# Kernel optimization log

Measured on AMD Instinct MI355X. Metric: run time of the kernel, lower is better.

Reference implementation:

```python
import jax, jax.numpy as jnp
import numpy as np

DIM, NH, WS, SS, MLP_RATIO = 192, 6, 8, 4, 4
EPS = 1e-5


def _rel_pos_index(ws):
    coords = np.stack(np.meshgrid(np.arange(ws), np.arange(ws), indexing='ij')).reshape(2, -1)
    rel = (coords[:, :, None] - coords[:, None, :]).transpose(1, 2, 0)
    rel[:, :, 0] += ws - 1
    rel[:, :, 1] += ws - 1
    rel[:, :, 0] *= 2 * ws - 1
    return rel.sum(-1)  # (ws*ws, ws*ws) int


def _attn_mask(hp, wp, ws, ss):
    img = np.zeros((hp, wp))
    slices = (slice(0, -ws), slice(-ws, -ss), slice(-ss, None))
    cnt = 0
    for hs in slices:
        for vs in slices:
            img[hs, vs] = cnt
            cnt += 1
    mw = img.reshape(hp // ws, ws, wp // ws, ws).transpose(0, 2, 1, 3).reshape(-1, ws * ws)
    am = mw[:, None, :] - mw[:, :, None]  # (nW, N, N)
    return jnp.asarray(np.where(am != 0, -100.0, 0.0).astype(np.float32))


def _ln(x, g, b):
    mu = jnp.mean(x, axis=-1, keepdims=True)
    var = jnp.mean(jnp.square(x - mu), axis=-1, keepdims=True)
    return (x - mu) * jax.lax.rsqrt(var + EPS) * g + b


def setup_inputs():
    key = jax.random.key(0)
    ks = jax.random.split(key, 8)
    B, H, W, C = 8, 128, 128, DIM
    hid = C * MLP_RATIO
    n = lambda k, s: jax.random.normal(k, s, dtype=jnp.float32) * 0.02
    return {
        'x': jax.random.normal(ks[0], (B, H * W, C), dtype=jnp.float32),
        'h': H, 'w': W,
        'norm1_g': jnp.ones((C,), jnp.float32), 'norm1_b': jnp.zeros((C,), jnp.float32),
        'qkv_w': n(ks[1], (C, 3 * C)), 'qkv_b': jnp.zeros((3 * C,), jnp.float32),
        'proj_w': n(ks[2], (C, C)), 'proj_b': jnp.zeros((C,), jnp.float32),
        'rel_bias_table': n(ks[3], ((2 * WS - 1) ** 2, NH)),
        'norm2_g': jnp.ones((C,), jnp.float32), 'norm2_b': jnp.zeros((C,), jnp.float32),
        'fc1_w': n(ks[4], (C, hid)), 'fc1_b': jnp.zeros((hid,), jnp.float32),
        'fc2_w': n(ks[5], (hid, C)), 'fc2_b': jnp.zeros((C,), jnp.float32),
    }


def reference(x, h, w, norm1_g, norm1_b, qkv_w, qkv_b, proj_w, proj_b,
              rel_bias_table, norm2_g, norm2_b, fc1_w, fc1_b, fc2_w, fc2_b):
    B, L, C = x.shape
    ws, ss, nh = WS, SS, NH
    hd = C // nh
    scale = hd ** (-0.5)

    shortcut = x
    xg = _ln(x, norm1_g, norm1_b).reshape(B, h, w, C)

    pad_h = (-h) % ws
    pad_w = (-w) % ws
    if pad_h or pad_w:
        xg = jnp.pad(xg, ((0, 0), (0, pad_h), (0, pad_w), (0, 0)))
    hp, wp = h + pad_h, w + pad_w
    if ss > 0:
        xg = jnp.roll(xg, (-ss, -ss), axis=(1, 2))

    # window partition -> (nB, N, C)
    win = xg.reshape(B, hp // ws, ws, wp // ws, ws, C).transpose(0, 1, 3, 2, 4, 5).reshape(-1, ws * ws, C)
    nB, N, _ = win.shape

    qkv = (win @ qkv_w + qkv_b).reshape(nB, N, 3, nh, hd).transpose(2, 0, 3, 1, 4)
    q, k, v = qkv[0] * scale, qkv[1], qkv[2]  # (nB, nh, N, hd)

    attn = jnp.einsum('bhnd,bhmd->bhnm', q, k)  # (nB, nh, N, N)
    rpi = _rel_pos_index(ws)
    bias = rel_bias_table[rpi.reshape(-1)].reshape(N, N, nh).transpose(2, 0, 1)
    attn = attn + bias[None]
    if ss > 0:
        mask = _attn_mask(hp, wp, ws, ss)  # (nW, N, N)
        nW = mask.shape[0]
        attn = (attn.reshape(nB // nW, nW, nh, N, N) + mask[None, :, None]).reshape(nB, nh, N, N)
    attn = jax.nn.softmax(attn, axis=-1)

    out = jnp.einsum('bhnm,bhmd->bnhd', attn, v).reshape(nB, N, C)
    out = out @ proj_w + proj_b

    # window reverse
    out = out.reshape(B, hp // ws, wp // ws, ws, ws, C).transpose(0, 1, 3, 2, 4, 5).reshape(B, hp, wp, C)
    if ss > 0:
        out = jnp.roll(out, (ss, ss), axis=(1, 2))
    out = out[:, :h, :w].reshape(B, h * w, C)

    x = shortcut + out
    xn2 = _ln(x, norm2_g, norm2_b)
    mlp = jax.nn.gelu(xn2 @ fc1_w + fc1_b, approximate=False) @ fc2_w + fc2_b
    return x + mlp
```

## Files before the change

### kernel.cpp

```cpp
#include <hip/hip_runtime.h>

typedef unsigned short u16;
typedef unsigned int   u32;
typedef __attribute__((ext_vector_type(8))) short bf16x8;
typedef __attribute__((ext_vector_type(4))) float f32x4;

#define L_TOK   16384
#define C_DIM   192
#define HID_DIM 768

#define OFF_QKV  0
#define OFF_PROJ 110592
#define OFF_FC1  147456
#define OFF_FC2  294912
#define CVT_TOT  442368

union FragU { int4 i4; bf16x8 h8; };

#define MFMA_B16(a,b,c) __builtin_amdgcn_mfma_f32_16x16x32_bf16(a,b,c,0,0,0)

__device__ __forceinline__ u16 f2bf(float f) {
    u32 t; __builtin_memcpy(&t, &f, 4);
    t += 0x7FFFu + ((t >> 16) & 1u);
    return (u16)(t >> 16);
}

__global__ __launch_bounds__(256) void k_cvt(
    const float* __restrict__ qkvw, const float* __restrict__ projw,
    const float* __restrict__ fc1w, const float* __restrict__ fc2w,
    u16* __restrict__ ws)
{
    const int i = blockIdx.x * 256 + threadIdx.x;
    if (i >= CVT_TOT) return;
    float v;
    if (i < OFF_PROJ) {
        const int k = i % 192, tmp = i / 192;
        const int cc = tmp % 96, head = tmp / 96;
        const int grp = cc >> 5, dim = cc & 31;
        v = qkvw[(size_t)k * 576 + grp * 192 + head * 32 + dim];
    } else if (i < OFF_FC1) {
        const int idx = i - OFF_PROJ;
        const int j = idx & 31, tmp = idx >> 5;
        const int c = tmp % 192, head = tmp / 192;
        v = projw[(size_t)(head * 32 + j) * 192 + c];
    } else if (i < OFF_FC2) {
        const int idx = i - OFF_FC1;
        const int k = idx % 192, h = idx / 192;
        v = fc1w[(size_t)k * 768 + h];
    } else {
        const int idx = i - OFF_FC2;
        const int h = idx % 768, c = idx / 768;
        v = fc2w[(size_t)h * 192 + c];
    }
    ws[i] = f2bf(v);
}

__global__ __launch_bounds__(256) void k_attnproj(
    const float* __restrict__ x, const float* __restrict__ g1v, const float* __restrict__ b1v,
    const u16* __restrict__ qkvwT, const float* __restrict__ qkvb,
    const float* __restrict__ relb, const u16* __restrict__ projT, const float* __restrict__ projb,
    float* __restrict__ x1)
{
    union SmemU {
        u16 xw[64 * 200];
        struct {
            u16 qsb[64 * 40];
            u16 ksb[64 * 40];
            u16 vsbT[32 * 72];
            u16 psb[64 * 72];
            u16 oh [64 * 40];
        } s;
    };
    __shared__ __align__(16) SmemU u;
    __shared__ __align__(16) u16 wbuf[192 * 40];
    __shared__ float relbs[225 * 6];

    const int wi = blockIdx.x;
    const int b  = wi >> 8;
    const int hb = (wi >> 4) & 15;
    const int wb = wi & 15;
    const int t  = threadIdx.x;
    const int lane = t & 63, w = t >> 6;
    const int l15 = lane & 15, quad = lane >> 4;
    const bool maskon = (hb == 15) || (wb == 15);
    const f32x4 zf = {0.f, 0.f, 0.f, 0.f};

    for (int i = t; i < 225 * 6; i += 256) relbs[i] = relb[i];

    {
        const int n  = t >> 2;
        const int q4 = t & 3;
        const int r = n >> 3, c = n & 7;
        const int ho = (hb * 8 + r + 4) & 127;
        const int wo = (wb * 8 + c + 4) & 127;
        const size_t xoff = ((size_t)b * L_TOK + ho * 128 + wo) * C_DIM;
        const float* xp = x + xoff + q4 * 48;
        float f[48];
        float sum = 0.f, sq = 0.f;
        #pragma unroll
        for (int i = 0; i < 12; ++i) {
            float4 v = *(const float4*)(xp + i * 4);
            f[i*4+0]=v.x; f[i*4+1]=v.y; f[i*4+2]=v.z; f[i*4+3]=v.w;
            sum += v.x+v.y+v.z+v.w;
            sq  += v.x*v.x + v.y*v.y + v.z*v.z + v.w*v.w;
        }
        sum += __shfl_xor(sum, 1); sum += __shfl_xor(sum, 2);
        sq  += __shfl_xor(sq, 1);  sq  += __shfl_xor(sq, 2);
        const float mu = sum * (1.f / 192.f);
        const float rstd = rsqrtf(sq * (1.f / 192.f) - mu * mu + 1e-5f);
        u16* xrow = u.xw + n * 200 + q4 * 48;
        #pragma unroll
        for (int i = 0; i < 6; ++i) {
            u32 pk[4];
            #pragma unroll
            for (int j = 0; j < 4; ++j) {
                float g0 = g1v[q4*48 + i*8 + j*2],     b0 = b1v[q4*48 + i*8 + j*2];
                float g1 = g1v[q4*48 + i*8 + j*2 + 1], b1 = b1v[q4*48 + i*8 + j*2 + 1];
                float y0 = (f[i*8+j*2]   - mu) * rstd * g0 + b0;
                float y1 = (f[i*8+j*2+1] - mu) * rstd * g1 + b1;
                pk[j] = (u32)f2bf(y0) | (((u32)f2bf(y1)) << 16);
            }
            *(int4*)(xrow + i * 8) = make_int4((int)pk[0], (int)pk[1], (int)pk[2], (int)pk[3]);
        }
    }
    __syncthreads();

    FragU afrag[6];
    #pragma unroll
    for (int kk = 0; kk < 6; ++kk)
        afrag[kk].i4 = *(const int4*)(u.xw + (w*16 + l15) * 200 + kk*32 + quad*8);

    const int qrow0 = w*16 + quad*4;

    f32x4 acc2[12];
    #pragma unroll
    for (int nt = 0; nt < 12; ++nt) acc2[nt] = zf;

    for (int head = 0; head < 6; ++head) {
        f32x4 accq[6];
        #pragma unroll
        for (int nt = 0; nt < 6; ++nt) accq[nt] = zf;

        for (int kc = 0; kc < 3; ++kc) {
            __syncthreads();
            {
                const u16* src = qkvwT + (size_t)head * (96 * 192) + kc * 64;
                #pragma unroll
                for (int i = 0; i < 3; ++i) {
                    const int e = t + i * 256;
                    const int cc = e >> 3, seg = e & 7;
                    *(int4*)(wbuf + cc*72 + seg*8) =
                        *(const int4*)(src + cc*192 + seg*8);
                }
            }
            __syncthreads();
            #pragma unroll
            for (int s = 0; s < 2; ++s) {
                #pragma unroll
                for (int nt = 0; nt < 6; ++nt) {
                    FragU bf_;
                    bf_.i4 = *(const int4*)(wbuf + (nt*16 + l15)*72 + s*32 + quad*8);
                    accq[nt] = MFMA_B16(afrag[kc*2 + s].h8, bf_.h8, accq[nt]);
                }
            }
        }
        #pragma unroll
        for (int nt = 0; nt < 6; ++nt) {
            const int grp = nt >> 1;
            const int dim = (nt & 1)*16 + l15;
            const float bias = qkvb[grp*192 + head*32 + dim];
            float vv[4];
            #pragma unroll
            for (int rg = 0; rg < 4; ++rg) vv[rg] = accq[nt][rg] + bias;
            if (grp == 0) {
                #pragma unroll
                for (int rg = 0; rg < 4; ++rg)
                    u.s.qsb[(qrow0 + rg)*40 + dim] = f2bf(vv[rg] * 0.17677669529663687f);
            } else if (grp == 1) {
                #pragma unroll
                for (int rg = 0; rg < 4; ++rg)
                    u.s.ksb[(qrow0 + rg)*40 + dim] = f2bf(vv[rg]);
            } else {
                u32 lo = (u32)f2bf(vv[0]) | (((u32)f2bf(vv[1])) << 16);
                u32 hi = (u32)f2bf(vv[2]) | (((u32)f2bf(vv[3])) << 16);
                *(uint2*)&u.s.vsbT[dim*72 + w*16 + quad*4] = make_uint2(lo, hi);
            }
        }
        __syncthreads();

        FragU qf; qf.i4 = *(const int4*)(u.s.qsb + (w*16 + l15)*40 + quad*8);
        f32x4 sv[4];
        #pragma unroll
        for (int nt = 0; nt < 4; ++nt) {
            FragU kf; kf.i4 = *(const int4*)(u.s.ksb + (nt*16 + l15)*40 + quad*8);
            sv[nt] = MFMA_B16(qf.h8, kf.h8, zf);
        }
        const int kr_ = l15 >> 3, kc2 = l15 & 7;
        #pragma unroll
        for (int rg = 0; rg < 4; ++rg) {
            const int qm = qrow0 + rg;
            const int qr = qm >> 3, qc = qm & 7;
            #pragma unroll
            for (int nt = 0; nt < 4; ++nt) {
                const int kr = nt*2 + kr_;
                sv[nt][rg] += relbs[((qr - kr + 7)*15 + (qc - kc2 + 7))*6 + head];
            }
        }
        if (maskon) {
            #pragma unroll
            for (int rg = 0; rg < 4; ++rg) {
                const int qm = qrow0 + rg;
                const int qr = qm >> 3, qc = qm & 7;
                const int regq = ((hb == 15) ? (qr < 4 ? 1 : 2) : 0) * 3
                               + ((wb == 15) ? (qc < 4 ? 1 : 2) : 0);
                #pragma unroll
                for (int nt = 0; nt < 4; ++nt) {
                    const int kr = nt*2 + kr_;
                    const int regk = ((hb == 15) ? (kr < 4 ? 1 : 2) : 0) * 3
                                   + ((wb == 15) ? (kc2 < 4 ? 1 : 2) : 0);
                    if (regq != regk) sv[nt][rg] -= 100.f;
                }
            }
        }
        #pragma unroll
        for (int rg = 0; rg < 4; ++rg) {
            float mx = fmaxf(fmaxf(sv[0][rg], sv[1][rg]), fmaxf(sv[2][rg], sv[3][rg]));
            mx = fmaxf(mx, __shfl_xor(mx, 1));
            mx = fmaxf(mx, __shfl_xor(mx, 2));
            mx = fmaxf(mx, __shfl_xor(mx, 4));
            mx = fmaxf(mx, __shfl_xor(mx, 8));
            float s0 = 0.f;
            #pragma unroll
            for (int nt = 0; nt < 4; ++nt) { sv[nt][rg] = __expf(sv[nt][rg] - mx); s0 += sv[nt][rg]; }
            s0 += __shfl_xor(s0, 1); s0 += __shfl_xor(s0, 2);
            s0 += __shfl_xor(s0, 4); s0 += __shfl_xor(s0, 8);
            const float inv = 1.f / s0;
            #pragma unroll
            for (int nt = 0; nt < 4; ++nt)
                u.s.psb[(qrow0 + rg)*72 + nt*16 + l15] = f2bf(sv[nt][rg] * inv);
        }

        FragU pa0, pa1;
        pa0.i4 = *(const int4*)(u.s.psb + (w*16 + l15)*72 + quad*8);
        pa1.i4 = *(const int4*)(u.s.psb + (w*16 + l15)*72 + 32 + quad*8);
        f32x4 ov[2];
        ov[0] = zf; ov[1] = zf;
        #pragma unroll
        for (int ntv = 0; ntv < 2; ++ntv) {
            FragU vb0, vb1;
            vb0.i4 = *(const int4*)(u.s.vsbT + (ntv*16 + l15)*72 + quad*8);
            vb1.i4 = *(const int4*)(u.s.vsbT + (ntv*16 + l15)*72 + 32 + quad*8);
            ov[ntv] = MFMA_B16(pa0.h8, vb0.h8, ov[ntv]);
            ov[ntv] = MFMA_B16(pa1.h8, vb1.h8, ov[ntv]);
        }
        #pragma unroll
        for (int ntv = 0; ntv < 2; ++ntv)
            #pragma unroll
            for (int rg = 0; rg < 4; ++rg)
                u.s.oh[(qrow0 + rg)*40 + ntv*16 + l15] = f2bf(ov[ntv][rg]);

        {
            const u16* src = projT + (size_t)head * (192 * 32);
            #pragma unroll
            for (int i = 0; i < 3; ++i) {
                const int e = t + i * 256;
                const int c = e >> 2, seg = e & 3;
                *(int4*)(wbuf + c*40 + seg*8) =
                    *(const int4*)(src + c*32 + seg*8);
            }
        }
        __syncthreads();
        FragU ao; ao.i4 = *(const int4*)(u.s.oh + (w*16 + l15)*40 + quad*8);
        #pragma unroll
        for (int nt = 0; nt < 12; ++nt) {
            FragU bp; bp.i4 = *(const int4*)(wbuf + (nt*16 + l15)*40 + quad*8);
            acc2[nt] = MFMA_B16(ao.h8, bp.h8, acc2[nt]);
        }
    }

    {
        float pb[12];
        #pragma unroll
        for (int nt = 0; nt < 12; ++nt) pb[nt] = projb[nt*16 + l15];
        #pragma unroll
        for (int rg = 0; rg < 4; ++rg) {
            const int tok = qrow0 + rg;
            const int tr = tok >> 3, tc = tok & 7;
            const int ho2 = (hb * 8 + tr + 4) & 127;
            const int wo2 = (wb * 8 + tc + 4) & 127;
            const size_t base = ((size_t)b * L_TOK + ho2 * 128 + wo2) * C_DIM;
            #pragma unroll
            for (int nt = 0; nt < 12; ++nt) {
                const int col = nt*16 + l15;
                x1[base + col] = acc2[nt][rg] + pb[nt] + x[base + col];
            }
        }
    }
}

__global__ __launch_bounds__(256, 2) void k_mlp(
    const float* x1, const float* __restrict__ g2v, const float* __restrict__ b2v,
    const u16* __restrict__ fc1wT, const float* __restrict__ fc1b,
    const u16* __restrict__ fc2wT, const float* __restrict__ fc2b,
    float* out)
{
    union SmemU {
        u16 xn[128 * 200];
        u16 hbuf[128 * 104];
    };
    __shared__ __align__(16) SmemU u;
    __shared__ __align__(16) u16 wT[192 * 40];

    const int blk = blockIdx.x;
    const int t = threadIdx.x;
    const size_t row0 = (size_t)blk * 128;
    const int lane = t & 63, w = t >> 6;
    const int l15 = lane & 15, quad = lane >> 4;
    const f32x4 zf = {0.f, 0.f, 0.f, 0.f};

    #pragma unroll
    for (int tk = 0; tk < 2; ++tk) {
        const int nn = t >> 2, q4 = t & 3;
        const int tok = tk * 64 + nn;
        const float* xp = x1 + (row0 + tok) * C_DIM + q4 * 48;
        float f[48];
        float sum = 0.f, sq = 0.f;
        #pragma unroll
        for (int i = 0; i < 12; ++i) {
            float4 v = *(const float4*)(xp + i * 4);
            f[i*4+0]=v.x; f[i*4+1]=v.y; f[i*4+2]=v.z; f[i*4+3]=v.w;
            sum += v.x+v.y+v.z+v.w;
            sq  += v.x*v.x + v.y*v.y + v.z*v.z + v.w*v.w;
        }
        sum += __shfl_xor(sum,1); sum += __shfl_xor(sum,2);
        sq  += __shfl_xor(sq,1);  sq  += __shfl_xor(sq,2);
        const float mu = sum * (1.f/192.f);
        const float rstd = rsqrtf(sq * (1.f/192.f) - mu*mu + 1e-5f);
        u16* xrow = u.xn + tok * 200 + q4 * 48;
        #pragma unroll
        for (int i = 0; i < 6; ++i) {
            u32 pk[4];
            #pragma unroll
            for (int j = 0; j < 4; ++j) {
                float g0 = g2v[q4*48 + i*8 + j*2],     b0 = b2v[q4*48 + i*8 + j*2];
                float g1 = g2v[q4*48 + i*8 + j*2 + 1], b1 = b2v[q4*48 + i*8 + j*2 + 1];
                float y0 = (f[i*8+j*2]   - mu) * rstd * g0 + b0;
                float y1 = (f[i*8+j*2+1] - mu) * rstd * g1 + b1;
                pk[j] = (u32)f2bf(y0) | (((u32)f2bf(y1)) << 16);
            }
            *(int4*)(xrow + i*8) = make_int4((int)pk[0], (int)pk[1], (int)pk[2], (int)pk[3]);
        }
    }
    __syncthreads();

    FragU afrag[2][6];
    #pragma unroll
    for (int mt = 0; mt < 2; ++mt)
        #pragma unroll
        for (int kk = 0; kk < 6; ++kk)
            afrag[mt][kk].i4 = *(const int4*)(u.xn + (mt*64 + w*16 + l15) * 200 + kk*32 + quad*8);

    f32x4 acc2[2][12];
    #pragma unroll
    for (int mt = 0; mt < 2; ++mt)
        #pragma unroll
        for (int nt = 0; nt < 12; ++nt) acc2[mt][nt] = zf;

    for (int hc = 0; hc < 8; ++hc) {
        f32x4 acc1[2][6];
        #pragma unroll
        for (int mt = 0; mt < 2; ++mt)
            #pragma unroll
            for (int nt = 0; nt < 6; ++nt) acc1[mt][nt] = zf;

        for (int kc = 0; kc < 3; ++kc) {
            __syncthreads();
            {
                const u16* src = fc1wT + (size_t)(hc * 96) * 192 + kc * 64;
                #pragma unroll
                for (int i = 0; i < 3; ++i) {
                    const int e = t + i * 256;
                    const int cc = e >> 3, seg = e & 7;
                    *(int4*)(wT + cc*72 + seg*8) =
                        *(const int4*)(src + cc*192 + seg*8);
                }
            }
            __syncthreads();
            #pragma unroll
            for (int s = 0; s < 2; ++s) {
                #pragma unroll
                for (int nt = 0; nt < 6; ++nt) {
                    FragU bf_;
                    bf_.i4 = *(const int4*)(wT + (nt*16 + l15)*72 + s*32 + quad*8);
                    acc1[0][nt] = MFMA_B16(afrag[0][kc*2 + s].h8, bf_.h8, acc1[0][nt]);
                    acc1[1][nt] = MFMA_B16(afrag[1][kc*2 + s].h8, bf_.h8, acc1[1][nt]);
                }
            }
        }
        #pragma unroll
        for (int nt = 0; nt < 6; ++nt) {
            const float bb = fc1b[hc*96 + nt*16 + l15];
            #pragma unroll
            for (int mt = 0; mt < 2; ++mt) {
                #pragma unroll
                for (int rg = 0; rg < 4; ++rg) {
                    float h = acc1[mt][nt][rg] + bb;
                    float g = 0.5f * h * (1.f + erff(h * 0.70710678118654752f));
                    u.hbuf[(mt*64 + w*16 + quad*4 + rg) * 104 + nt*16 + l15] = f2bf(g);
                }
            }
        }
        for (int sc = 0; sc < 3; ++sc) {
            __syncthreads();
            {
                const u16* src = fc2wT + hc * 96 + sc * 32;
                #pragma unroll
                for (int i = 0; i < 3; ++i) {
                    const int e = t + i * 256;
                    const int c = e >> 2, seg = e & 3;
                    *(int4*)(wT + c*40 + seg*8) =
                        *(const int4*)(src + c*768 + seg*8);
                }
            }
            __syncthreads();
            FragU ha0, ha1;
            ha0.i4 = *(const int4*)(u.hbuf + (w*16 + l15) * 104 + sc*32 + quad*8);
            ha1.i4 = *(const int4*)(u.hbuf + (64 + w*16 + l15) * 104 + sc*32 + quad*8);
            #pragma unroll
            for (int nt = 0; nt < 12; ++nt) {
                FragU bf_;
                bf_.i4 = *(const int4*)(wT + (nt*16 + l15)*40 + quad*8);
                acc2[0][nt] = MFMA_B16(ha0.h8, bf_.h8, acc2[0][nt]);
                acc2[1][nt] = MFMA_B16(ha1.h8, bf_.h8, acc2[1][nt]);
            }
        }
    }

    #pragma unroll
    for (int nt = 0; nt < 12; ++nt) {
        const int col = nt*16 + l15;
        const float bb = fc2b[col];
        #pragma unroll
        for (int mt = 0; mt < 2; ++mt) {
            #pragma unroll
            for (int rg = 0; rg < 4; ++rg) {
                const size_t idx = (row0 + mt*64 + w*16 + quad*4 + rg) * C_DIM + col;
                out[idx] = acc2[mt][nt][rg] + bb + x1[idx];
            }
        }
    }
}

extern "C" void kernel_launch(void* const* d_in, const int* in_sizes, int n_in,
                              void* d_out, int out_size, void* d_ws, size_t ws_size,
                              hipStream_t stream) {
    const float* x     = (const float*)d_in[0];
    const float* g1v   = (const float*)d_in[3];
    const float* b1v   = (const float*)d_in[4];
    const float* qkvw  = (const float*)d_in[5];
    const float* qkvb  = (const float*)d_in[6];
    const float* projw = (const float*)d_in[7];
    const float* projb = (const float*)d_in[8];
    const float* relb  = (const float*)d_in[9];
    const float* g2v   = (const float*)d_in[10];
    const float* b2v   = (const float*)d_in[11];
    const float* fc1w  = (const float*)d_in[12];
    const float* fc1b  = (const float*)d_in[13];
    const float* fc2w  = (const float*)d_in[14];
    const float* fc2b  = (const float*)d_in[15];

    float* x1 = (float*)d_out;
    u16* wsb  = (u16*)d_ws;

    hipLaunchKernelGGL(k_cvt, dim3((CVT_TOT + 255) / 256), dim3(256), 0, stream,
                       qkvw, projw, fc1w, fc2w, wsb);
    hipLaunchKernelGGL(k_attnproj, dim3(2048), dim3(256), 0, stream,
                       x, g1v, b1v, wsb + OFF_QKV, qkvb, relb, wsb + OFF_PROJ, projb, x1);
    hipLaunchKernelGGL(k_mlp, dim3(1024), dim3(256), 0, stream,
                       x1, g2v, b2v, wsb + OFF_FC1, fc1b, wsb + OFF_FC2, fc2b, x1);
}
```

Baseline: 601.5 us.

## Process two windows per attention block to reuse staged weights

Each attention block now handles two 64-token windows: each wave covers 32 rows (two M-tiles) instead of 16, and the grid is halved. Every qkv and proj weight tile staged into shared memory is therefore reused across twice as many tokens, which cuts global weight traffic and barrier count per token. The cost is higher register pressure, since the accumulators and fragments double (launch bounds now request 2 blocks per CU), plus a larger shared-memory footprint and fewer blocks in the grid.

```diff
diff --git a/kernel.cpp b/kernel.cpp
--- a/kernel.cpp
+++ b/kernel.cpp
@@ -55,45 +55,52 @@
     ws[i] = f2bf(v);
 }
 
-__global__ __launch_bounds__(256) void k_attnproj(
+__global__ __launch_bounds__(256, 2) void k_attnproj(
     const float* __restrict__ x, const float* __restrict__ g1v, const float* __restrict__ b1v,
     const u16* __restrict__ qkvwT, const float* __restrict__ qkvb,
     const float* __restrict__ relb, const u16* __restrict__ projT, const float* __restrict__ projb,
     float* __restrict__ x1)
 {
+    struct PW {
+        u16 qsb[64 * 40];
+        u16 ksb[64 * 40];
+        u16 vsbT[32 * 72];
+        u16 psb[64 * 72];
+        u16 oh [64 * 40];
+    };
     union SmemU {
-        u16 xw[64 * 200];
-        struct {
-            u16 qsb[64 * 40];
-            u16 ksb[64 * 40];
-            u16 vsbT[32 * 72];
-            u16 psb[64 * 72];
-            u16 oh [64 * 40];
-        } s;
+        u16 xw[128 * 200];
+        PW pw[2];
     };
     __shared__ __align__(16) SmemU u;
     __shared__ __align__(16) u16 wbuf[192 * 40];
     __shared__ float relbs[225 * 6];
 
-    const int wi = blockIdx.x;
-    const int b  = wi >> 8;
-    const int hb = (wi >> 4) & 15;
-    const int wb = wi & 15;
     const int t  = threadIdx.x;
     const int lane = t & 63, w = t >> 6;
+    const int win = w >> 1, half = w & 1;
     const int l15 = lane & 15, quad = lane >> 4;
+    const int wi2 = blockIdx.x * 2 + win;
+    const int b  = wi2 >> 8;
+    const int hb = (wi2 >> 4) & 15;
+    const int wb = wi2 & 15;
     const bool maskon = (hb == 15) || (wb == 15);
     const f32x4 zf = {0.f, 0.f, 0.f, 0.f};
 
     for (int i = t; i < 225 * 6; i += 256) relbs[i] = relb[i];
 
-    {
-        const int n  = t >> 2;
-        const int q4 = t & 3;
+    #pragma unroll
+    for (int tk = 0; tk < 2; ++tk) {
+        const int nn = t >> 2, q4 = t & 3;
+        const int tok = tk * 64 + nn;
+        const int tw = tok >> 6, n = tok & 63;
+        const int wiA = blockIdx.x * 2 + tw;
+        const int bA  = wiA >> 8;
+        const int hbA = (wiA >> 4) & 15, wbA = wiA & 15;
         const int r = n >> 3, c = n & 7;
-        const int ho = (hb * 8 + r + 4) & 127;
-        const int wo = (wb * 8 + c + 4) & 127;
-        const size_t xoff = ((size_t)b * L_TOK + ho * 128 + wo) * C_DIM;
+        const int ho = (hbA * 8 + r + 4) & 127;
+        const int wo = (wbA * 8 + c + 4) & 127;
+        const size_t xoff = ((size_t)bA * L_TOK + ho * 128 + wo) * C_DIM;
         const float* xp = x + xoff + q4 * 48;
         float f[48];
         float sum = 0.f, sq = 0.f;
@@ -108,7 +115,7 @@
         sq  += __shfl_xor(sq, 1);  sq  += __shfl_xor(sq, 2);
         const float mu = sum * (1.f / 192.f);
         const float rstd = rsqrtf(sq * (1.f / 192.f) - mu * mu + 1e-5f);
-        u16* xrow = u.xw + n * 200 + q4 * 48;
+        u16* xrow = u.xw + tok * 200 + q4 * 48;
         #pragma unroll
         for (int i = 0; i < 6; ++i) {
             u32 pk[4];
@@ -125,21 +132,29 @@
     }
     __syncthreads();
 
-    FragU afrag[6];
-    #pragma unroll
-    for (int kk = 0; kk < 6; ++kk)
-        afrag[kk].i4 = *(const int4*)(u.xw + (w*16 + l15) * 200 + kk*32 + quad*8);
-
-    const int qrow0 = w*16 + quad*4;
-
-    f32x4 acc2[12];
-    #pragma unroll
-    for (int nt = 0; nt < 12; ++nt) acc2[nt] = zf;
+    FragU afrag[2][6];
+    #pragma unroll
+    for (int mt = 0; mt < 2; ++mt)
+        #pragma unroll
+        for (int kk = 0; kk < 6; ++kk)
+            afrag[mt][kk].i4 = *(const int4*)(u.xw +
+                (win*64 + half*32 + mt*16 + l15) * 200 + kk*32 + quad*8);
+
+    PW* P = &u.pw[win];
+    const int rb = half*32 + quad*4;
+
+    f32x4 acc2[2][12];
+    #pragma unroll
+    for (int mt = 0; mt < 2; ++mt)
+        #pragma unroll
+        for (int nt = 0; nt < 12; ++nt) acc2[mt][nt] = zf;
 
     for (int head = 0; head < 6; ++head) {
-        f32x4 accq[6];
-        #pragma unroll
-        for (int nt = 0; nt < 6; ++nt) accq[nt] = zf;
+        f32x4 accq[2][6];
+        #pragma unroll
+        for (int mt = 0; mt < 2; ++mt)
+            #pragma unroll
+            for (int nt = 0; nt < 6; ++nt) accq[mt][nt] = zf;
 
         for (int kc = 0; kc < 3; ++kc) {
             __syncthreads();
@@ -160,104 +175,128 @@
                 for (int nt = 0; nt < 6; ++nt) {
                     FragU bf_;
                     bf_.i4 = *(const int4*)(wbuf + (nt*16 + l15)*72 + s*32 + quad*8);
-                    accq[nt] = MFMA_B16(afrag[kc*2 + s].h8, bf_.h8, accq[nt]);
-                }
-            }
-        }
-        #pragma unroll
-        for (int nt = 0; nt < 6; ++nt) {
-            const int grp = nt >> 1;
-            const int dim = (nt & 1)*16 + l15;
-            const float bias = qkvb[grp*192 + head*32 + dim];
-            float vv[4];
-            #pragma unroll
-            for (int rg = 0; rg < 4; ++rg) vv[rg] = accq[nt][rg] + bias;
-            if (grp == 0) {
-                #pragma unroll
-                for (int rg = 0; rg < 4; ++rg)
-                    u.s.qsb[(qrow0 + rg)*40 + dim] = f2bf(vv[rg] * 0.17677669529663687f);
-            } else if (grp == 1) {
-                #pragma unroll
-                for (int rg = 0; rg < 4; ++rg)
-                    u.s.ksb[(qrow0 + rg)*40 + dim] = f2bf(vv[rg]);
-            } else {
-                u32 lo = (u32)f2bf(vv[0]) | (((u32)f2bf(vv[1])) << 16);
-                u32 hi = (u32)f2bf(vv[2]) | (((u32)f2bf(vv[3])) << 16);
-                *(uint2*)&u.s.vsbT[dim*72 + w*16 + quad*4] = make_uint2(lo, hi);
+                    accq[0][nt] = MFMA_B16(afrag[0][kc*2 + s].h8, bf_.h8, accq[0][nt]);
+                    accq[1][nt] = MFMA_B16(afrag[1][kc*2 + s].h8, bf_.h8, accq[1][nt]);
+                }
+            }
+        }
+        #pragma unroll
+        for (int mt = 0; mt < 2; ++mt) {
+            #pragma unroll
+            for (int nt = 0; nt < 6; ++nt) {
+                const int grp = nt >> 1;
+                const int dim = (nt & 1)*16 + l15;
+                const float bias = qkvb[grp*192 + head*32 + dim];
+                float vv[4];
+                #pragma unroll
+                for (int rg = 0; rg < 4; ++rg) vv[rg] = accq[mt][nt][rg] + bias;
+                const int rowb = rb + mt*16;
+                if (grp == 0) {
+                    #pragma unroll
+                    for (int rg = 0; rg < 4; ++rg)
+                        P->qsb[(rowb + rg)*40 + dim] = f2bf(vv[rg] * 0.17677669529663687f);
+                } else if (grp == 1) {
+                    #pragma unroll
+                    for (int rg = 0; rg < 4; ++rg)
+                        P->ksb[(rowb + rg)*40 + dim] = f2bf(vv[rg]);
+                } else {
+                    u32 lo = (u32)f2bf(vv[0]) | (((u32)f2bf(vv[1])) << 16);
+                    u32 hi = (u32)f2bf(vv[2]) | (((u32)f2bf(vv[3])) << 16);
+                    *(uint2*)&P->vsbT[dim*72 + rowb] = make_uint2(lo, hi);
+                }
             }
         }
         __syncthreads();
 
-        FragU qf; qf.i4 = *(const int4*)(u.s.qsb + (w*16 + l15)*40 + quad*8);
-        f32x4 sv[4];
+        FragU qf0, qf1;
+        qf0.i4 = *(const int4*)(P->qsb + (half*32 + l15)*40 + quad*8);
+        qf1.i4 = *(const int4*)(P->qsb + (half*32 + 16 + l15)*40 + quad*8);
+        f32x4 sv[2][4];
         #pragma unroll
         for (int nt = 0; nt < 4; ++nt) {
-            FragU kf; kf.i4 = *(const int4*)(u.s.ksb + (nt*16 + l15)*40 + quad*8);
-            sv[nt] = MFMA_B16(qf.h8, kf.h8, zf);
+            FragU kf; kf.i4 = *(const int4*)(P->ksb + (nt*16 + l15)*40 + quad*8);
+            sv[0][nt] = MFMA_B16(qf0.h8, kf.h8, zf);
+            sv[1][nt] = MFMA_B16(qf1.h8, kf.h8, zf);
         }
         const int kr_ = l15 >> 3, kc2 = l15 & 7;
         #pragma unroll
-        for (int rg = 0; rg < 4; ++rg) {
-            const int qm = qrow0 + rg;
-            const int qr = qm >> 3, qc = qm & 7;
-            #pragma unroll
-            for (int nt = 0; nt < 4; ++nt) {
-                const int kr = nt*2 + kr_;
-                sv[nt][rg] += relbs[((qr - kr + 7)*15 + (qc - kc2 + 7))*6 + head];
-            }
-        }
-        if (maskon) {
+        for (int mt = 0; mt < 2; ++mt) {
             #pragma unroll
             for (int rg = 0; rg < 4; ++rg) {
-                const int qm = qrow0 + rg;
+                const int qm = rb + mt*16 + rg;
                 const int qr = qm >> 3, qc = qm & 7;
-                const int regq = ((hb == 15) ? (qr < 4 ? 1 : 2) : 0) * 3
-                               + ((wb == 15) ? (qc < 4 ? 1 : 2) : 0);
                 #pragma unroll
                 for (int nt = 0; nt < 4; ++nt) {
                     const int kr = nt*2 + kr_;
-                    const int regk = ((hb == 15) ? (kr < 4 ? 1 : 2) : 0) * 3
-                                   + ((wb == 15) ? (kc2 < 4 ? 1 : 2) : 0);
-                    if (regq != regk) sv[nt][rg] -= 100.f;
-                }
-            }
-        }
-        #pragma unroll
-        for (int rg = 0; rg < 4; ++rg) {
-            float mx = fmaxf(fmaxf(sv[0][rg], sv[1][rg]), fmaxf(sv[2][rg], sv[3][rg]));
-            mx = fmaxf(mx, __shfl_xor(mx, 1));
-            mx = fmaxf(mx, __shfl_xor(mx, 2));
-            mx = fmaxf(mx, __shfl_xor(mx, 4));
-            mx = fmaxf(mx, __shfl_xor(mx, 8));
-            float s0 = 0.f;
-            #pragma unroll
-            for (int nt = 0; nt < 4; ++nt) { sv[nt][rg] = __expf(sv[nt][rg] - mx); s0 += sv[nt][rg]; }
-            s0 += __shfl_xor(s0, 1); s0 += __shfl_xor(s0, 2);
-            s0 += __shfl_xor(s0, 4); s0 += __shfl_xor(s0, 8);
-            const float inv = 1.f / s0;
-            #pragma unroll
-            for (int nt = 0; nt < 4; ++nt)
-                u.s.psb[(qrow0 + rg)*72 + nt*16 + l15] = f2bf(sv[nt][rg] * inv);
-        }
-
-        FragU pa0, pa1;
-        pa0.i4 = *(const int4*)(u.s.psb + (w*16 + l15)*72 + quad*8);
-        pa1.i4 = *(const int4*)(u.s.psb + (w*16 + l15)*72 + 32 + quad*8);
-        f32x4 ov[2];
-        ov[0] = zf; ov[1] = zf;
+                    sv[mt][nt][rg] += relbs[((qr - kr + 7)*15 + (qc - kc2 + 7))*6 + head];
+                }
+            }
+        }
+        if (maskon) {
+            #pragma unroll
+            for (int mt = 0; mt < 2; ++mt) {
+                #pragma unroll
+                for (int rg = 0; rg < 4; ++rg) {
+                    const int qm = rb + mt*16 + rg;
+                    const int qr = qm >> 3, qc = qm & 7;
+                    const int regq = ((hb == 15) ? (qr < 4 ? 1 : 2) : 0) * 3
+                                   + ((wb == 15) ? (qc < 4 ? 1 : 2) : 0);
+                    #pragma unroll
+                    for (int nt = 0; nt < 4; ++nt) {
+                        const int kr = nt*2 + kr_;
+                        const int regk = ((hb == 15) ? (kr < 4 ? 1 : 2) : 0) * 3
+                                       + ((wb == 15) ? (kc2 < 4 ? 1 : 2) : 0);
+                        if (regq != regk) sv[mt][nt][rg] -= 100.f;
+                    }
+                }
+            }
+        }
+        #pragma unroll
+        for (int mt = 0; mt < 2; ++mt) {
+            #pragma unroll
+            for (int rg = 0; rg < 4; ++rg) {
+                float mx = fmaxf(fmaxf(sv[mt][0][rg], sv[mt][1][rg]),
+                                 fmaxf(sv[mt][2][rg], sv[mt][3][rg]));
+                mx = fmaxf(mx, __shfl_xor(mx, 1));
+                mx = fmaxf(mx, __shfl_xor(mx, 2));
+                mx = fmaxf(mx, __shfl_xor(mx, 4));
+                mx = fmaxf(mx, __shfl_xor(mx, 8));
+                float s0 = 0.f;
+                #pragma unroll
+                for (int nt = 0; nt < 4; ++nt) {
+                    sv[mt][nt][rg] = __expf(sv[mt][nt][rg] - mx); s0 += sv[mt][nt][rg];
+                }
+                s0 += __shfl_xor(s0, 1); s0 += __shfl_xor(s0, 2);
+                s0 += __shfl_xor(s0, 4); s0 += __shfl_xor(s0, 8);
+                const float inv = 1.f / s0;
+                #pragma unroll
+                for (int nt = 0; nt < 4; ++nt)
+                    P->psb[(rb + mt*16 + rg)*72 + nt*16 + l15] = f2bf(sv[mt][nt][rg] * inv);
+            }
+        }
+
+        FragU vb[2][2];
         #pragma unroll
         for (int ntv = 0; ntv < 2; ++ntv) {
-            FragU vb0, vb1;
-            vb0.i4 = *(const int4*)(u.s.vsbT + (ntv*16 + l15)*72 + quad*8);
-            vb1.i4 = *(const int4*)(u.s.vsbT + (ntv*16 + l15)*72 + 32 + quad*8);
-            ov[ntv] = MFMA_B16(pa0.h8, vb0.h8, ov[ntv]);
-            ov[ntv] = MFMA_B16(pa1.h8, vb1.h8, ov[ntv]);
-        }
-        #pragma unroll
-        for (int ntv = 0; ntv < 2; ++ntv)
-            #pragma unroll
-            for (int rg = 0; rg < 4; ++rg)
-                u.s.oh[(qrow0 + rg)*40 + ntv*16 + l15] = f2bf(ov[ntv][rg]);
+            vb[ntv][0].i4 = *(const int4*)(P->vsbT + (ntv*16 + l15)*72 + quad*8);
+            vb[ntv][1].i4 = *(const int4*)(P->vsbT + (ntv*16 + l15)*72 + 32 + quad*8);
+        }
+        #pragma unroll
+        for (int mt = 0; mt < 2; ++mt) {
+            FragU pa0, pa1;
+            pa0.i4 = *(const int4*)(P->psb + (half*32 + mt*16 + l15)*72 + quad*8);
+            pa1.i4 = *(const int4*)(P->psb + (half*32 + mt*16 + l15)*72 + 32 + quad*8);
+            f32x4 ov0 = zf, ov1 = zf;
+            ov0 = MFMA_B16(pa0.h8, vb[0][0].h8, ov0);
+            ov0 = MFMA_B16(pa1.h8, vb[0][1].h8, ov0);
+            ov1 = MFMA_B16(pa0.h8, vb[1][0].h8, ov1);
+            ov1 = MFMA_B16(pa1.h8, vb[1][1].h8, ov1);
+            #pragma unroll
+            for (int rg = 0; rg < 4; ++rg) {
+                P->oh[(rb + mt*16 + rg)*40 + l15]      = f2bf(ov0[rg]);
+                P->oh[(rb + mt*16 + rg)*40 + 16 + l15] = f2bf(ov1[rg]);
+            }
+        }
 
         {
             const u16* src = projT + (size_t)head * (192 * 32);
@@ -270,11 +309,14 @@
             }
         }
         __syncthreads();
-        FragU ao; ao.i4 = *(const int4*)(u.s.oh + (w*16 + l15)*40 + quad*8);
+        FragU ao0, ao1;
+        ao0.i4 = *(const int4*)(P->oh + (half*32 + l15)*40 + quad*8);
+        ao1.i4 = *(const int4*)(P->oh + (half*32 + 16 + l15)*40 + quad*8);
         #pragma unroll
         for (int nt = 0; nt < 12; ++nt) {
             FragU bp; bp.i4 = *(const int4*)(wbuf + (nt*16 + l15)*40 + quad*8);
-            acc2[nt] = MFMA_B16(ao.h8, bp.h8, acc2[nt]);
+            acc2[0][nt] = MFMA_B16(ao0.h8, bp.h8, acc2[0][nt]);
+            acc2[1][nt] = MFMA_B16(ao1.h8, bp.h8, acc2[1][nt]);
         }
     }
 
@@ -283,16 +325,19 @@
         #pragma unroll
         for (int nt = 0; nt < 12; ++nt) pb[nt] = projb[nt*16 + l15];
         #pragma unroll
-        for (int rg = 0; rg < 4; ++rg) {
-            const int tok = qrow0 + rg;
-            const int tr = tok >> 3, tc = tok & 7;
-            const int ho2 = (hb * 8 + tr + 4) & 127;
-            const int wo2 = (wb * 8 + tc + 4) & 127;
-            const size_t base = ((size_t)b * L_TOK + ho2 * 128 + wo2) * C_DIM;
-            #pragma unroll
-            for (int nt = 0; nt < 12; ++nt) {
-                const int col = nt*16 + l15;
-                x1[base + col] = acc2[nt][rg] + pb[nt] + x[base + col];
+        for (int mt = 0; mt < 2; ++mt) {
+            #pragma unroll
+            for (int rg = 0; rg < 4; ++rg) {
+                const int tok = rb + mt*16 + rg;
+                const int tr = tok >> 3, tc = tok & 7;
+                const int ho2 = (hb * 8 + tr + 4) & 127;
+                const int wo2 = (wb * 8 + tc + 4) & 127;
+                const size_t base = ((size_t)b * L_TOK + ho2 * 128 + wo2) * C_DIM;
+                #pragma unroll
+                for (int nt = 0; nt < 12; ++nt) {
+                    const int col = nt*16 + l15;
+                    x1[base + col] = acc2[mt][nt][rg] + pb[nt] + x[base + col];
+                }
             }
         }
     }
@@ -474,7 +519,7 @@
 
     hipLaunchKernelGGL(k_cvt, dim3((CVT_TOT + 255) / 256), dim3(256), 0, stream,
                        qkvw, projw, fc1w, fc2w, wsb);
-    hipLaunchKernelGGL(k_attnproj, dim3(2048), dim3(256), 0, stream,
+    hipLaunchKernelGGL(k_attnproj, dim3(1024), dim3(256), 0, stream,
                        x, g1v, b1v, wsb + OFF_QKV, qkvb, relb, wsb + OFF_PROJ, projb, x1);
     hipLaunchKernelGGL(k_mlp, dim3(1024), dim3(256), 0, stream,
                        x1, g2v, b2v, wsb + OFF_FC1, fc1b, wsb + OFF_FC2, fc2b, x1);
```

After: 557.8 us. 7.3% less time.
